# Kernel tuning notes

Measured on AMD Instinct MI355X. Metric: run time of the kernel, lower is better.

The kernel has to match this reference:

```python
import jax, jax.numpy as jnp
import numpy as np

N = 100000      # num zones (nodes)
E = 1600000     # num edges
IN = 16         # in_channels
HID = 128       # hidden_dim
HEADS = 4
C = HID // HEADS  # 32, per-head channels of gat1
NEG = 0.2       # PyG GATConv negative_slope default
LN_EPS = 1e-5


def setup_inputs() -> dict:
    key = jax.random.key(0)
    ks = jax.random.split(key, 14)
    x = jax.random.normal(ks[0], (N, IN), jnp.float32)
    edge_index = jax.random.randint(ks[1], (2, E), 0, N, dtype=jnp.int32)
    # --- GATConv layer 1: in=IN, heads=HEADS, out=C, concat=True ---
    W1 = jax.random.normal(ks[2], (IN, HEADS * C), jnp.float32) / np.sqrt(IN)
    a_src1 = jax.random.normal(ks[3], (HEADS, C), jnp.float32) / np.sqrt(C)
    a_dst1 = jax.random.normal(ks[4], (HEADS, C), jnp.float32) / np.sqrt(C)
    b1 = jnp.zeros((HEADS * C,), jnp.float32)
    # --- LayerNorm 1 ---
    g1 = jnp.ones((HID,), jnp.float32)
    beta1 = jnp.zeros((HID,), jnp.float32)
    # --- GATConv layer 2: in=HID, heads=1, out=HID, concat=False ---
    W2 = jax.random.normal(ks[5], (HID, HID), jnp.float32) / np.sqrt(HID)
    a_src2 = jax.random.normal(ks[6], (1, HID), jnp.float32) / np.sqrt(HID)
    a_dst2 = jax.random.normal(ks[7], (1, HID), jnp.float32) / np.sqrt(HID)
    b2 = jnp.zeros((HID,), jnp.float32)
    # --- LayerNorm 2 ---
    g2 = jnp.ones((HID,), jnp.float32)
    beta2 = jnp.zeros((HID,), jnp.float32)
    return dict(x=x, edge_index=edge_index, W1=W1, a_src1=a_src1, a_dst1=a_dst1,
                b1=b1, g1=g1, beta1=beta1, W2=W2, a_src2=a_src2, a_dst2=a_dst2,
                b2=b2, g2=g2, beta2=beta2)


def gat_conv(x, src, dst, W, a_src, a_dst, b, heads, ch, concat):
    """PyG GATConv (eval mode, no edge_attr), self-loops already in src/dst."""
    n = x.shape[0]
    h = (x @ W).reshape(n, heads, ch)                    # [N,H,C]
    alpha_src = jnp.einsum('nhc,hc->nh', h, a_src)       # [N,H]
    alpha_dst = jnp.einsum('nhc,hc->nh', h, a_dst)       # [N,H]
    e = jax.nn.leaky_relu(alpha_src[src] + alpha_dst[dst], NEG)  # [Etot,H]
    # segment softmax over destination node
    m = jax.ops.segment_max(e, dst, num_segments=n)      # [N,H]
    ex = jnp.exp(e - m[dst])
    denom = jax.ops.segment_sum(ex, dst, num_segments=n) # [N,H]
    alpha = ex / denom[dst]                              # [Etot,H]
    msg = h[src] * alpha[..., None]                      # [Etot,H,C]
    out = jax.ops.segment_sum(msg, dst, num_segments=n)  # [N,H,C]
    out = out.reshape(n, heads * ch) if concat else out.mean(axis=1)
    return out + b


def layer_norm(x, g, b):
    mu = x.mean(-1, keepdims=True)
    var = ((x - mu) ** 2).mean(-1, keepdims=True)
    return (x - mu) * jax.lax.rsqrt(var + LN_EPS) * g + b


def reference(x, edge_index, W1, a_src1, a_dst1, b1, g1, beta1,
              W2, a_src2, a_dst2, b2, g2, beta2):
    loops = jnp.arange(N, dtype=edge_index.dtype)
    src = jnp.concatenate([edge_index[0], loops])
    dst = jnp.concatenate([edge_index[1], loops])
    h = gat_conv(x, src, dst, W1, a_src1, a_dst1, b1, HEADS, C, concat=True)
    h = layer_norm(jax.nn.elu(h), g1, beta1)
    h = gat_conv(h, src, dst, W2, a_src2, a_dst2, b2, 1, HID, concat=False)
    h = layer_norm(jax.nn.elu(h), g2, beta2)
    return h
```

## Files before the change

kernel.cpp:

```cpp
#include <hip/hip_runtime.h>

#define IN_CH 16
#define HID 128
#define HEADS 4
#define NEG 0.2f
#define LN_EPS 1e-5f
#define BCAP 8192

typedef short bf16x8 __attribute__((ext_vector_type(8)));
typedef float f32x4 __attribute__((ext_vector_type(4)));

__device__ __forceinline__ float bf2f(unsigned short u) {
  return __uint_as_float(((unsigned)u) << 16);
}
__device__ __forceinline__ float bflo(unsigned u) {
  return __uint_as_float(u << 16);
}
__device__ __forceinline__ float bfhi(unsigned u) {
  return __uint_as_float(u & 0xffff0000u);
}
__device__ __forceinline__ unsigned short f2bf(float f) {
  unsigned u = __float_as_uint(f);
  unsigned r = (u + 0x7fffu + ((u >> 16) & 1u)) >> 16;
  return (unsigned short)r;
}
__device__ __forceinline__ float sb(unsigned v, int sh) {
  return (float)((int)(v << (24 - sh)) >> 24);
}

__global__ __launch_bounds__(128) void k_gemm1(
    const float* __restrict__ x, const float* __restrict__ W1,
    const float* __restrict__ a_src, const float* __restrict__ a_dst,
    signed char* __restrict__ hq, float* __restrict__ rec,
    float* __restrict__ adst, int N) {
  int n = blockIdx.x;
  int c = threadIdx.x;
  __shared__ float xs[IN_CH];
  __shared__ float wmax[2];
  if (c < IN_CH) xs[c] = x[n * IN_CH + c];
  __syncthreads();
  float acc = 0.f;
#pragma unroll
  for (int k = 0; k < IN_CH; ++k) acc += xs[k] * W1[k * HID + c];
  float av = acc * a_src[c];
  float dv = acc * a_dst[c];
#pragma unroll
  for (int o = 16; o > 0; o >>= 1) {
    av += __shfl_down(av, o, 32);
    dv += __shfl_down(dv, o, 32);
  }
  if ((c & 31) == 0) {
    rec[n * 8 + (c >> 5)] = av;
    adst[n * HEADS + (c >> 5)] = dv;
  }
  float m = fabsf(acc);
#pragma unroll
  for (int o = 32; o > 0; o >>= 1) m = fmaxf(m, __shfl_xor(m, o, 64));
  if ((c & 63) == 0) wmax[c >> 6] = m;
  __syncthreads();
  float mm = fmaxf(wmax[0], wmax[1]);
  float rs = (mm > 0.f) ? 127.f / mm : 0.f;
  hq[(size_t)n * HID + c] = (signed char)__float2int_rn(acc * rs);
  if (c == 0) rec[n * 8 + 4] = mm * (1.f / 127.f);
}

__global__ __launch_bounds__(256) void k_hist(
    const int* __restrict__ ei, int E, int Etot, int NBK, int NBLK,
    int* __restrict__ bcnt) {
  __shared__ int lh[512];
  int blk = blockIdx.x;
  for (int i = threadIdx.x; i < 512; i += 256) lh[i] = 0;
  __syncthreads();
  int s0 = blk * 8192, s1 = min(s0 + 8192, Etot);
  for (int e = s0 + threadIdx.x; e < s1; e += 256) {
    int d = (e < E) ? ei[E + e] : (e - E);
    atomicAdd(&lh[d >> 8], 1);
  }
  __syncthreads();
  for (int i = threadIdx.x; i < NBK; i += 256) bcnt[i * NBLK + blk] = lh[i];
}

__global__ __launch_bounds__(256) void k_scan1(
    const int* __restrict__ deg, int* __restrict__ part, int* __restrict__ aux,
    int N) {
  int i = blockIdx.x * 256 + threadIdx.x;
  int v = (i < N) ? deg[i] : 0;
  int lane = threadIdx.x & 63, w = threadIdx.x >> 6;
  int inc = v;
#pragma unroll
  for (int o = 1; o < 64; o <<= 1) {
    int t = __shfl_up(inc, o, 64);
    if (lane >= o) inc += t;
  }
  __shared__ int wsum[4];
  if (lane == 63) wsum[w] = inc;
  __syncthreads();
  int woff = 0;
#pragma unroll
  for (int k = 0; k < 4; ++k)
    if (k < w) woff += wsum[k];
  if (i < N) part[i] = woff + inc - v;
  if (threadIdx.x == 255) aux[blockIdx.x] = woff + inc;
}

__global__ __launch_bounds__(512) void k_scan2(int* __restrict__ aux, int nb) {
  int i = threadIdx.x;
  int v = (i < nb) ? aux[i] : 0;
  int lane = i & 63, w = i >> 6;
  int inc = v;
#pragma unroll
  for (int o = 1; o < 64; o <<= 1) {
    int t = __shfl_up(inc, o, 64);
    if (lane >= o) inc += t;
  }
  __shared__ int wsum[8];
  if (lane == 63) wsum[w] = inc;
  __syncthreads();
  int woff = 0;
#pragma unroll
  for (int k = 0; k < 8; ++k)
    if (k < w) woff += wsum[k];
  if (i < nb) aux[i] = woff + inc - v;
}

__global__ __launch_bounds__(256) void k_scan3g(
    const int* __restrict__ part, const int* __restrict__ aux,
    int* __restrict__ out, int M) {
  int i = blockIdx.x * 256 + threadIdx.x;
  if (i < M) out[i] = part[i] + aux[blockIdx.x];
}

__global__ __launch_bounds__(256) void k_bucket(
    const int* __restrict__ ei, const int* __restrict__ bpre, int E, int Etot,
    int NBK, int NBLK, unsigned* __restrict__ bbuf) {
  __shared__ int lc[512];
  int blk = blockIdx.x;
  for (int i = threadIdx.x; i < NBK; i += 256) lc[i] = bpre[i * NBLK + blk];
  __syncthreads();
  int s0 = blk * 8192, s1 = min(s0 + 8192, Etot);
  for (int e = s0 + threadIdx.x; e < s1; e += 256) {
    int d = (e < E) ? ei[E + e] : (e - E);
    int s = (e < E) ? ei[e] : d;
    int pos = atomicAdd(&lc[d >> 8], 1);
    bbuf[pos] = ((unsigned)s << 8) | (unsigned)(d & 255);
  }
}

__global__ __launch_bounds__(256) void k_build(
    const unsigned* __restrict__ bbuf, const int* __restrict__ bpre,
    int* __restrict__ rowstart, int* __restrict__ csr_src, int N, int Etot,
    int NBK, int NBLK) {
  __shared__ int ldeg[256], lcur[256], wsum[4];
  __shared__ int lout[BCAP];
  int bin = blockIdx.x;
  int base = bpre[bin * NBLK];
  int next = (bin + 1 < NBK) ? bpre[(bin + 1) * NBLK] : Etot;
  int cnt = next - base;
  if (cnt > BCAP) cnt = BCAP;
  int tid = threadIdx.x;
  ldeg[tid] = 0;
  __syncthreads();
  for (int i = tid; i < cnt; i += 256)
    atomicAdd(&ldeg[bbuf[base + i] & 255u], 1);
  __syncthreads();
  int v = ldeg[tid];
  int lane = tid & 63, wv = tid >> 6;
  int inc = v;
#pragma unroll
  for (int o = 1; o < 64; o <<= 1) {
    int t = __shfl_up(inc, o, 64);
    if (lane >= o) inc += t;
  }
  if (lane == 63) wsum[wv] = inc;
  __syncthreads();
  int woff = 0;
#pragma unroll
  for (int k = 0; k < 4; ++k)
    if (k < wv) woff += wsum[k];
  int pre = woff + inc - v;
  int node = bin * 256 + tid;
  if (node < N) rowstart[node] = base + pre;
  lcur[tid] = pre;
  __syncthreads();
  for (int i = tid; i < cnt; i += 256) {
    unsigned u = bbuf[base + i];
    int p = atomicAdd(&lcur[u & 255u], 1);
    lout[p] = (int)(u >> 8);
  }
  __syncthreads();
  for (int i = tid; i < cnt; i += 256) csr_src[base + i] = lout[i];
  if (bin == 0 && tid == 0) rowstart[N] = Etot;
}

__global__ __launch_bounds__(256) void k_agg1(
    const int* __restrict__ rowstart, const int* __restrict__ csr_src,
    const float* __restrict__ rec, const float* __restrict__ adst,
    const signed char* __restrict__ hq, const float* __restrict__ bias,
    const float* __restrict__ g, const float* __restrict__ beta,
    unsigned short* __restrict__ outb, int N) {
  int d = blockIdx.x * 16 + (threadIdx.x >> 4);
  if (d >= N) return;
  int lane = threadIdx.x & 15;
  int c0 = lane << 3;
  int hd = lane >> 2;
  float ad = adst[d * HEADS + hd];
  int beg = rowstart[d], end = rowstart[d + 1];
  float a0 = 0.f, a1 = 0.f, a2 = 0.f, a3 = 0.f;
  float a4 = 0.f, a5 = 0.f, a6 = 0.f, a7 = 0.f, wsum = 0.f;
  for (int i = beg; i < end; i += 8) {
    int s[8];
#pragma unroll
    for (int j = 0; j < 8; ++j) {
      int e = i + j;
      s[j] = csr_src[e < end ? e : end - 1];
    }
    float lg[8], sc[8];
    uint2 p[8];
#pragma unroll
    for (int j = 0; j < 8; ++j) {
      lg[j] = rec[s[j] * 8 + hd];
      sc[j] = rec[s[j] * 8 + 4];
    }
#pragma unroll
    for (int j = 0; j < 8; ++j)
      p[j] = *(const uint2*)(hq + (size_t)s[j] * HID + c0);
#pragma unroll
    for (int j = 0; j < 8; ++j) {
      float v = lg[j] + ad;
      v = v < 0.f ? NEG * v : v;
      float ex = __expf(v);
      float w = (i + j < end) ? ex : 0.f;
      wsum += w;
      float ws = w * sc[j];
      a0 += ws * sb(p[j].x, 0);
      a1 += ws * sb(p[j].x, 8);
      a2 += ws * sb(p[j].x, 16);
      a3 += ws * sb(p[j].x, 24);
      a4 += ws * sb(p[j].y, 0);
      a5 += ws * sb(p[j].y, 8);
      a6 += ws * sb(p[j].y, 16);
      a7 += ws * sb(p[j].y, 24);
    }
  }
  float rw = 1.f / wsum;
  float v0 = a0 * rw + bias[c0 + 0];
  float v1 = a1 * rw + bias[c0 + 1];
  float v2 = a2 * rw + bias[c0 + 2];
  float v3 = a3 * rw + bias[c0 + 3];
  float v4 = a4 * rw + bias[c0 + 4];
  float v5 = a5 * rw + bias[c0 + 5];
  float v6 = a6 * rw + bias[c0 + 6];
  float v7 = a7 * rw + bias[c0 + 7];
  v0 = v0 > 0.f ? v0 : (__expf(v0) - 1.f);
  v1 = v1 > 0.f ? v1 : (__expf(v1) - 1.f);
  v2 = v2 > 0.f ? v2 : (__expf(v2) - 1.f);
  v3 = v3 > 0.f ? v3 : (__expf(v3) - 1.f);
  v4 = v4 > 0.f ? v4 : (__expf(v4) - 1.f);
  v5 = v5 > 0.f ? v5 : (__expf(v5) - 1.f);
  v6 = v6 > 0.f ? v6 : (__expf(v6) - 1.f);
  v7 = v7 > 0.f ? v7 : (__expf(v7) - 1.f);
  float s1 = ((v0 + v1) + (v2 + v3)) + ((v4 + v5) + (v6 + v7));
  float s2 = ((v0 * v0 + v1 * v1) + (v2 * v2 + v3 * v3)) +
             ((v4 * v4 + v5 * v5) + (v6 * v6 + v7 * v7));
#pragma unroll
  for (int o = 8; o > 0; o >>= 1) {
    s1 += __shfl_down(s1, o, 16);
    s2 += __shfl_down(s2, o, 16);
  }
  s1 = __shfl(s1, 0, 16);
  s2 = __shfl(s2, 0, 16);
  float mu = s1 * (1.f / HID);
  float var = s2 * (1.f / HID) - mu * mu;
  float inv = rsqrtf(var + LN_EPS);
  ushort4 q0, q1;
  q0.x = f2bf((v0 - mu) * inv * g[c0 + 0] + beta[c0 + 0]);
  q0.y = f2bf((v1 - mu) * inv * g[c0 + 1] + beta[c0 + 1]);
  q0.z = f2bf((v2 - mu) * inv * g[c0 + 2] + beta[c0 + 2]);
  q0.w = f2bf((v3 - mu) * inv * g[c0 + 3] + beta[c0 + 3]);
  q1.x = f2bf((v4 - mu) * inv * g[c0 + 4] + beta[c0 + 4]);
  q1.y = f2bf((v5 - mu) * inv * g[c0 + 5] + beta[c0 + 5]);
  q1.z = f2bf((v6 - mu) * inv * g[c0 + 6] + beta[c0 + 6]);
  q1.w = f2bf((v7 - mu) * inv * g[c0 + 7] + beta[c0 + 7]);
  *(ushort4*)(outb + (size_t)d * HID + c0) = q0;
  *(ushort4*)(outb + (size_t)d * HID + c0 + 4) = q1;
}

__global__ __launch_bounds__(256) void k_agg2(
    const int* __restrict__ rowstart, const int* __restrict__ csr_src,
    const float* __restrict__ asrc, const float* __restrict__ adst,
    const unsigned short* __restrict__ hb, const float* __restrict__ bias,
    const float* __restrict__ g, const float* __restrict__ beta,
    float* __restrict__ out, int N) {
  int d = blockIdx.x * 16 + (threadIdx.x >> 4);
  if (d >= N) return;
  int lane = threadIdx.x & 15;
  int c0 = lane << 3;
  float ad = adst[d];
  int beg = rowstart[d], end = rowstart[d + 1];
  float a0 = 0.f, a1 = 0.f, a2 = 0.f, a3 = 0.f;
  float a4 = 0.f, a5 = 0.f, a6 = 0.f, a7 = 0.f, wsum = 0.f;
  for (int i = beg; i < end; i += 8) {
    int s[8];
#pragma unroll
    for (int j = 0; j < 8; ++j) {
      int e = i + j;
      s[j] = csr_src[e < end ? e : end - 1];
    }
    float lg[8];
    uint4 p[8];
#pragma unroll
    for (int j = 0; j < 8; ++j) lg[j] = asrc[s[j]];
#pragma unroll
    for (int j = 0; j < 8; ++j)
      p[j] = *(const uint4*)(hb + (size_t)s[j] * HID + c0);
    float wv[8];
#pragma unroll
    for (int j = 0; j < 8; ++j) {
      float v = lg[j] + ad;
      v = v < 0.f ? NEG * v : v;
      float ex = __expf(v);
      wv[j] = (i + j < end) ? ex : 0.f;
    }
    wsum += ((wv[0] + wv[1]) + (wv[2] + wv[3])) +
            ((wv[4] + wv[5]) + (wv[6] + wv[7]));
#pragma unroll
    for (int j = 0; j < 8; ++j) {
      a0 += wv[j] * bflo(p[j].x);
      a1 += wv[j] * bfhi(p[j].x);
      a2 += wv[j] * bflo(p[j].y);
      a3 += wv[j] * bfhi(p[j].y);
      a4 += wv[j] * bflo(p[j].z);
      a5 += wv[j] * bfhi(p[j].z);
      a6 += wv[j] * bflo(p[j].w);
      a7 += wv[j] * bfhi(p[j].w);
    }
  }
  float rw = 1.f / wsum;
  float v0 = a0 * rw + bias[c0 + 0];
  float v1 = a1 * rw + bias[c0 + 1];
  float v2 = a2 * rw + bias[c0 + 2];
  float v3 = a3 * rw + bias[c0 + 3];
  float v4 = a4 * rw + bias[c0 + 4];
  float v5 = a5 * rw + bias[c0 + 5];
  float v6 = a6 * rw + bias[c0 + 6];
  float v7 = a7 * rw + bias[c0 + 7];
  v0 = v0 > 0.f ? v0 : (__expf(v0) - 1.f);
  v1 = v1 > 0.f ? v1 : (__expf(v1) - 1.f);
  v2 = v2 > 0.f ? v2 : (__expf(v2) - 1.f);
  v3 = v3 > 0.f ? v3 : (__expf(v3) - 1.f);
  v4 = v4 > 0.f ? v4 : (__expf(v4) - 1.f);
  v5 = v5 > 0.f ? v5 : (__expf(v5) - 1.f);
  v6 = v6 > 0.f ? v6 : (__expf(v6) - 1.f);
  v7 = v7 > 0.f ? v7 : (__expf(v7) - 1.f);
  float s1 = ((v0 + v1) + (v2 + v3)) + ((v4 + v5) + (v6 + v7));
  float s2 = ((v0 * v0 + v1 * v1) + (v2 * v2 + v3 * v3)) +
             ((v4 * v4 + v5 * v5) + (v6 * v6 + v7 * v7));
#pragma unroll
  for (int o = 8; o > 0; o >>= 1) {
    s1 += __shfl_down(s1, o, 16);
    s2 += __shfl_down(s2, o, 16);
  }
  s1 = __shfl(s1, 0, 16);
  s2 = __shfl(s2, 0, 16);
  float mu = s1 * (1.f / HID);
  float var = s2 * (1.f / HID) - mu * mu;
  float inv = rsqrtf(var + LN_EPS);
  float4 o0, o1;
  o0.x = (v0 - mu) * inv * g[c0 + 0] + beta[c0 + 0];
  o0.y = (v1 - mu) * inv * g[c0 + 1] + beta[c0 + 1];
  o0.z = (v2 - mu) * inv * g[c0 + 2] + beta[c0 + 2];
  o0.w = (v3 - mu) * inv * g[c0 + 3] + beta[c0 + 3];
  o1.x = (v4 - mu) * inv * g[c0 + 4] + beta[c0 + 4];
  o1.y = (v5 - mu) * inv * g[c0 + 5] + beta[c0 + 5];
  o1.z = (v6 - mu) * inv * g[c0 + 6] + beta[c0 + 6];
  o1.w = (v7 - mu) * inv * g[c0 + 7] + beta[c0 + 7];
  *(float4*)(out + (size_t)d * HID + c0) = o0;
  *(float4*)(out + (size_t)d * HID + c0 + 4) = o1;
}

__global__ __launch_bounds__(256) void k_w2pack(
    const float* __restrict__ W2, unsigned short* __restrict__ w2hi,
    unsigned short* __restrict__ w2lo) {
  int idx = blockIdx.x * 256 + threadIdx.x;
  int i = idx & 7;
  int lane = (idx >> 3) & 63;
  int t = (idx >> 9) & 7;
  int kb = idx >> 12;
  int k = kb * 32 + (lane >> 4) * 8 + i;
  int c = t * 16 + (lane & 15);
  float w = W2[k * HID + c];
  unsigned short hi = f2bf(w);
  float res = w - bf2f(hi);
  w2hi[idx] = hi;
  w2lo[idx] = f2bf(res);
}

__global__ __launch_bounds__(256) void k_gemm2m(
    const unsigned short* __restrict__ x2b,
    const unsigned short* __restrict__ w2hi,
    const unsigned short* __restrict__ w2lo,
    const float* __restrict__ a_src, const float* __restrict__ a_dst,
    unsigned short* __restrict__ h2b, float* __restrict__ asrc,
    float* __restrict__ adst, int N) {
  __shared__ float cs[4][16][132];
  int w = threadIdx.x >> 6;
  int l = threadIdx.x & 63;
  int n0 = blockIdx.x * 128 + w * 32;
  int m = l & 15;
  int kg = l >> 4;
  int naA = n0 + m;
  if (naA >= N) naA = N - 1;
  int naB = n0 + 16 + m;
  if (naB >= N) naB = N - 1;
  const unsigned short* xA = x2b + (size_t)naA * HID + kg * 8;
  const unsigned short* xB = x2b + (size_t)naB * HID + kg * 8;
  f32x4 accA[8] = {};
  f32x4 accB[8] = {};
#pragma unroll
  for (int kb = 0; kb < 4; ++kb) {
    bf16x8 aA = *(const bf16x8*)(xA + kb * 32);
    bf16x8 aB = *(const bf16x8*)(xB + kb * 32);
#pragma unroll
    for (int t = 0; t < 8; ++t) {
      bf16x8 bl = *(const bf16x8*)(w2lo + ((kb * 8 + t) * 64 + l) * 8);
      bf16x8 bh = *(const bf16x8*)(w2hi + ((kb * 8 + t) * 64 + l) * 8);
      accA[t] = __builtin_amdgcn_mfma_f32_16x16x32_bf16(aA, bl, accA[t], 0, 0, 0);
      accA[t] = __builtin_amdgcn_mfma_f32_16x16x32_bf16(aA, bh, accA[t], 0, 0, 0);
      accB[t] = __builtin_amdgcn_mfma_f32_16x16x32_bf16(aB, bl, accB[t], 0, 0, 0);
      accB[t] = __builtin_amdgcn_mfma_f32_16x16x32_bf16(aB, bh, accB[t], 0, 0, 0);
    }
  }
  auto epilog = [&](const f32x4(&acc)[8], int noff) {
#pragma unroll
    for (int t = 0; t < 8; ++t)
#pragma unroll
      for (int j = 0; j < 4; ++j) cs[w][kg * 4 + j][t * 16 + m] = acc[t][j];
    __syncthreads();
    int r2 = l & 15;
    int q = l >> 4;
    int n = n0 + noff + r2;
    if (n < N) {
      const float* rowp = &cs[w][r2][0];
      float pa = 0.f, pd = 0.f;
#pragma unroll
      for (int j = 0; j < 8; ++j) {
        int cc = q * 32 + j * 4;
        float4 v = *(const float4*)(rowp + cc);
        float4 as = *(const float4*)(a_src + cc);
        float4 av = *(const float4*)(a_dst + cc);
        pa += v.x * as.x + v.y * as.y + v.z * as.z + v.w * as.w;
        pd += v.x * av.x + v.y * av.y + v.z * av.z + v.w * av.w;
        ushort4 ob;
        ob.x = f2bf(v.x);
        ob.y = f2bf(v.y);
        ob.z = f2bf(v.z);
        ob.w = f2bf(v.w);
        *(ushort4*)(h2b + (size_t)n * HID + cc) = ob;
      }
      pa += __shfl_xor(pa, 16, 64);
      pa += __shfl_xor(pa, 32, 64);
      pd += __shfl_xor(pd, 16, 64);
      pd += __shfl_xor(pd, 32, 64);
      if (q == 0) {
        asrc[n] = pa;
        adst[n] = pd;
      }
    }
    __syncthreads();
  };
  epilog(accA, 0);
  epilog(accB, 16);
}

extern "C" void kernel_launch(void* const* d_in, const int* in_sizes, int n_in,
                              void* d_out, int out_size, void* d_ws, size_t ws_size,
                              hipStream_t stream) {
  const float* x      = (const float*)d_in[0];
  const int*   ei     = (const int*)d_in[1];
  const float* W1     = (const float*)d_in[2];
  const float* a_src1 = (const float*)d_in[3];
  const float* a_dst1 = (const float*)d_in[4];
  const float* b1     = (const float*)d_in[5];
  const float* g1     = (const float*)d_in[6];
  const float* beta1  = (const float*)d_in[7];
  const float* W2     = (const float*)d_in[8];
  const float* a_src2 = (const float*)d_in[9];
  const float* a_dst2 = (const float*)d_in[10];
  const float* b2     = (const float*)d_in[11];
  const float* g2     = (const float*)d_in[12];
  const float* beta2  = (const float*)d_in[13];
  float* out = (float*)d_out;

  const int N = in_sizes[0] / IN_CH;
  const int E = in_sizes[1] / 2;
  const int Etot = E + N;

  const int NBK = (N + 255) >> 8;
  const int NBLK = (Etot + 8191) >> 13;
  const int M = NBK * NBLK;
  const int Mblk = (M + 255) / 256;

  unsigned char* U = (unsigned char*)d_ws;
  signed char* hq = (signed char*)U;
  float* rec = (float*)(U + (size_t)N * HID);
  unsigned short* x2b =
      (unsigned short*)(U + (size_t)N * HID + (size_t)N * 32);
  unsigned short* h2b = x2b + (size_t)N * HID;
  float* adst1 = (float*)(h2b + (size_t)N * HID);
  float* asrc2 = adst1 + (size_t)N * HEADS;
  float* adst2 = asrc2 + N;
  int* rowstart = (int*)(adst2 + N);
  int* aux      = rowstart + N + 4;
  int* bcnt     = aux + 1024;
  int* bpart    = bcnt + M;
  int* bpre     = bpart + M;
  unsigned* bbuf = (unsigned*)(bpre + M);
  int* csr_src  = (int*)(bbuf + Etot);
  unsigned short* w2hi = (unsigned short*)(csr_src + Etot);
  unsigned short* w2lo = w2hi + 16384;

  k_w2pack<<<64, 256, 0, stream>>>(W2, w2hi, w2lo);

  k_hist<<<NBLK, 256, 0, stream>>>(ei, E, Etot, NBK, NBLK, bcnt);
  k_scan1<<<Mblk, 256, 0, stream>>>(bcnt, bpart, aux, M);
  k_scan2<<<1, 512, 0, stream>>>(aux, Mblk);
  k_scan3g<<<Mblk, 256, 0, stream>>>(bpart, aux, bpre, M);
  k_bucket<<<NBLK, 256, 0, stream>>>(ei, bpre, E, Etot, NBK, NBLK, bbuf);
  k_build<<<NBK, 256, 0, stream>>>(bbuf, bpre, rowstart, csr_src, N, Etot,
                                   NBK, NBLK);

  k_gemm1<<<N, 128, 0, stream>>>(x, W1, a_src1, a_dst1, hq, rec, adst1, N);
  k_agg1<<<(N + 15) / 16, 256, 0, stream>>>(rowstart, csr_src, rec, adst1, hq,
                                            b1, g1, beta1, x2b, N);

  k_gemm2m<<<(N + 127) / 128, 256, 0, stream>>>(x2b, w2hi, w2lo, a_src2,
                                                a_dst2, h2b, asrc2, adst2, N);
  k_agg2<<<(N + 15) / 16, 256, 0, stream>>>(rowstart, csr_src, asrc2, adst2,
                                            h2b, b2, g2, beta2, out, N);
}
```

Baseline: 357.4 us.

## Quantize layer-2 features to int8 with per-node scale and batch gemm1 nodes

Layer-2 projected features are now stored as int8 with a per-node absmax scale, packed alongside the source attention logit in a float2. This replaces bf16 storage and halves the bytes gathered per edge in the second aggregation. Separately, gemm1 now handles 8 nodes per block, with W1 staged in shared memory and float4 math, instead of one 128-thread block per node. The int8 quantization lowers precision of the layer-2 messages, which risks larger numerical error in the output.

```diff
diff --git a/kernel.cpp b/kernel.cpp
--- a/kernel.cpp
+++ b/kernel.cpp
@@ -28,40 +28,64 @@
   return (float)((int)(v << (24 - sh)) >> 24);
 }
 
-__global__ __launch_bounds__(128) void k_gemm1(
+__global__ __launch_bounds__(256) void k_gemm1(
     const float* __restrict__ x, const float* __restrict__ W1,
     const float* __restrict__ a_src, const float* __restrict__ a_dst,
     signed char* __restrict__ hq, float* __restrict__ rec,
     float* __restrict__ adst, int N) {
-  int n = blockIdx.x;
-  int c = threadIdx.x;
-  __shared__ float xs[IN_CH];
-  __shared__ float wmax[2];
-  if (c < IN_CH) xs[c] = x[n * IN_CH + c];
-  __syncthreads();
-  float acc = 0.f;
-#pragma unroll
-  for (int k = 0; k < IN_CH; ++k) acc += xs[k] * W1[k * HID + c];
-  float av = acc * a_src[c];
-  float dv = acc * a_dst[c];
-#pragma unroll
-  for (int o = 16; o > 0; o >>= 1) {
-    av += __shfl_down(av, o, 32);
-    dv += __shfl_down(dv, o, 32);
-  }
-  if ((c & 31) == 0) {
-    rec[n * 8 + (c >> 5)] = av;
-    adst[n * HEADS + (c >> 5)] = dv;
-  }
-  float m = fabsf(acc);
-#pragma unroll
-  for (int o = 32; o > 0; o >>= 1) m = fmaxf(m, __shfl_xor(m, o, 64));
-  if ((c & 63) == 0) wmax[c >> 6] = m;
-  __syncthreads();
-  float mm = fmaxf(wmax[0], wmax[1]);
-  float rs = (mm > 0.f) ? 127.f / mm : 0.f;
-  hq[(size_t)n * HID + c] = (signed char)__float2int_rn(acc * rs);
-  if (c == 0) rec[n * 8 + 4] = mm * (1.f / 127.f);
+  __shared__ float w1s[IN_CH][HID];
+  __shared__ float xsh[8][IN_CH];
+  int tid = threadIdx.x;
+  int nb = blockIdx.x * 8;
+  for (int i = tid; i < IN_CH * HID; i += 256) ((float*)w1s)[i] = W1[i];
+  if (tid < 128) {
+    int nl = tid >> 4, k = tid & 15;
+    int n = nb + nl;
+    xsh[nl][k] = (n < N) ? x[n * IN_CH + k] : 0.f;
+  }
+  __syncthreads();
+  int nl = tid >> 5;
+  int l32 = tid & 31;
+  int c0 = l32 << 2;
+  int n = nb + nl;
+  float4 acc = make_float4(0.f, 0.f, 0.f, 0.f);
+#pragma unroll
+  for (int k = 0; k < IN_CH; ++k) {
+    float xv = xsh[nl][k];
+    float4 wv = *(const float4*)(&w1s[k][c0]);
+    acc.x += xv * wv.x;
+    acc.y += xv * wv.y;
+    acc.z += xv * wv.z;
+    acc.w += xv * wv.w;
+  }
+  float4 as4 = *(const float4*)(a_src + c0);
+  float4 ad4 = *(const float4*)(a_dst + c0);
+  float av = acc.x * as4.x + acc.y * as4.y + acc.z * as4.z + acc.w * as4.w;
+  float dv = acc.x * ad4.x + acc.y * ad4.y + acc.z * ad4.z + acc.w * ad4.w;
+  av += __shfl_xor(av, 1);
+  av += __shfl_xor(av, 2);
+  av += __shfl_xor(av, 4);
+  dv += __shfl_xor(dv, 1);
+  dv += __shfl_xor(dv, 2);
+  dv += __shfl_xor(dv, 4);
+  float m = fmaxf(fmaxf(fabsf(acc.x), fabsf(acc.y)),
+                  fmaxf(fabsf(acc.z), fabsf(acc.w)));
+#pragma unroll
+  for (int o = 1; o < 32; o <<= 1) m = fmaxf(m, __shfl_xor(m, o));
+  if (n < N) {
+    float rs = (m > 0.f) ? 127.f / m : 0.f;
+    int b0 = __float2int_rn(acc.x * rs) & 255;
+    int b1 = __float2int_rn(acc.y * rs) & 255;
+    int b2 = __float2int_rn(acc.z * rs) & 255;
+    int b3 = __float2int_rn(acc.w * rs) & 255;
+    *(unsigned*)(hq + (size_t)n * HID + c0) =
+        (unsigned)(b0 | (b1 << 8) | (b2 << 16) | (b3 << 24));
+    if ((l32 & 7) == 0) {
+      rec[n * 8 + (l32 >> 3)] = av;
+      adst[n * HEADS + (l32 >> 3)] = dv;
+    }
+    if (l32 == 0) rec[n * 8 + 4] = m * (1.f / 127.f);
+  }
 }
 
 __global__ __launch_bounds__(256) void k_hist(
@@ -287,8 +311,8 @@
 
 __global__ __launch_bounds__(256) void k_agg2(
     const int* __restrict__ rowstart, const int* __restrict__ csr_src,
-    const float* __restrict__ asrc, const float* __restrict__ adst,
-    const unsigned short* __restrict__ hb, const float* __restrict__ bias,
+    const float2* __restrict__ rec2, const float* __restrict__ adst,
+    const signed char* __restrict__ hq2, const float* __restrict__ bias,
     const float* __restrict__ g, const float* __restrict__ beta,
     float* __restrict__ out, int N) {
   int d = blockIdx.x * 16 + (threadIdx.x >> 4);
@@ -306,33 +330,29 @@
       int e = i + j;
       s[j] = csr_src[e < end ? e : end - 1];
     }
-    float lg[8];
-    uint4 p[8];
-#pragma unroll
-    for (int j = 0; j < 8; ++j) lg[j] = asrc[s[j]];
+    float2 r[8];
+    uint2 p[8];
+#pragma unroll
+    for (int j = 0; j < 8; ++j) r[j] = rec2[s[j]];
 #pragma unroll
     for (int j = 0; j < 8; ++j)
-      p[j] = *(const uint4*)(hb + (size_t)s[j] * HID + c0);
-    float wv[8];
+      p[j] = *(const uint2*)(hq2 + (size_t)s[j] * HID + c0);
 #pragma unroll
     for (int j = 0; j < 8; ++j) {
-      float v = lg[j] + ad;
+      float v = r[j].x + ad;
       v = v < 0.f ? NEG * v : v;
       float ex = __expf(v);
-      wv[j] = (i + j < end) ? ex : 0.f;
-    }
-    wsum += ((wv[0] + wv[1]) + (wv[2] + wv[3])) +
-            ((wv[4] + wv[5]) + (wv[6] + wv[7]));
-#pragma unroll
-    for (int j = 0; j < 8; ++j) {
-      a0 += wv[j] * bflo(p[j].x);
-      a1 += wv[j] * bfhi(p[j].x);
-      a2 += wv[j] * bflo(p[j].y);
-      a3 += wv[j] * bfhi(p[j].y);
-      a4 += wv[j] * bflo(p[j].z);
-      a5 += wv[j] * bfhi(p[j].z);
-      a6 += wv[j] * bflo(p[j].w);
-      a7 += wv[j] * bfhi(p[j].w);
+      float w = (i + j < end) ? ex : 0.f;
+      wsum += w;
+      float ws = w * r[j].y;
+      a0 += ws * sb(p[j].x, 0);
+      a1 += ws * sb(p[j].x, 8);
+      a2 += ws * sb(p[j].x, 16);
+      a3 += ws * sb(p[j].x, 24);
+      a4 += ws * sb(p[j].y, 0);
+      a5 += ws * sb(p[j].y, 8);
+      a6 += ws * sb(p[j].y, 16);
+      a7 += ws * sb(p[j].y, 24);
     }
   }
   float rw = 1.f / wsum;
@@ -400,7 +420,7 @@
     const unsigned short* __restrict__ w2hi,
     const unsigned short* __restrict__ w2lo,
     const float* __restrict__ a_src, const float* __restrict__ a_dst,
-    unsigned short* __restrict__ h2b, float* __restrict__ asrc,
+    signed char* __restrict__ hq2, float2* __restrict__ rec2,
     float* __restrict__ adst, int N) {
   __shared__ float cs[4][16][132];
   int w = threadIdx.x >> 6;
@@ -439,30 +459,43 @@
     int r2 = l & 15;
     int q = l >> 4;
     int n = n0 + noff + r2;
+    const float* rowp = &cs[w][r2][0];
+    float4 v[8];
+    float pa = 0.f, pd = 0.f, mx = 0.f;
+#pragma unroll
+    for (int j = 0; j < 8; ++j) {
+      int cc = q * 32 + j * 4;
+      v[j] = *(const float4*)(rowp + cc);
+      float4 as = *(const float4*)(a_src + cc);
+      float4 av = *(const float4*)(a_dst + cc);
+      pa += v[j].x * as.x + v[j].y * as.y + v[j].z * as.z + v[j].w * as.w;
+      pd += v[j].x * av.x + v[j].y * av.y + v[j].z * av.z + v[j].w * av.w;
+      mx = fmaxf(mx, fmaxf(fmaxf(fabsf(v[j].x), fabsf(v[j].y)),
+                           fmaxf(fabsf(v[j].z), fabsf(v[j].w))));
+    }
+    pa += __shfl_xor(pa, 16);
+    pa += __shfl_xor(pa, 32);
+    pd += __shfl_xor(pd, 16);
+    pd += __shfl_xor(pd, 32);
+    mx = fmaxf(mx, __shfl_xor(mx, 16));
+    mx = fmaxf(mx, __shfl_xor(mx, 32));
     if (n < N) {
-      const float* rowp = &cs[w][r2][0];
-      float pa = 0.f, pd = 0.f;
+      float rs = (mx > 0.f) ? 127.f / mx : 0.f;
+      unsigned u[8];
 #pragma unroll
       for (int j = 0; j < 8; ++j) {
-        int cc = q * 32 + j * 4;
-        float4 v = *(const float4*)(rowp + cc);
-        float4 as = *(const float4*)(a_src + cc);
-        float4 av = *(const float4*)(a_dst + cc);
-        pa += v.x * as.x + v.y * as.y + v.z * as.z + v.w * as.w;
-        pd += v.x * av.x + v.y * av.y + v.z * av.z + v.w * av.w;
-        ushort4 ob;
-        ob.x = f2bf(v.x);
-        ob.y = f2bf(v.y);
-        ob.z = f2bf(v.z);
-        ob.w = f2bf(v.w);
-        *(ushort4*)(h2b + (size_t)n * HID + cc) = ob;
+        int b0 = __float2int_rn(v[j].x * rs) & 255;
+        int b1 = __float2int_rn(v[j].y * rs) & 255;
+        int b2 = __float2int_rn(v[j].z * rs) & 255;
+        int b3 = __float2int_rn(v[j].w * rs) & 255;
+        u[j] = (unsigned)(b0 | (b1 << 8) | (b2 << 16) | (b3 << 24));
       }
-      pa += __shfl_xor(pa, 16, 64);
-      pa += __shfl_xor(pa, 32, 64);
-      pd += __shfl_xor(pd, 16, 64);
-      pd += __shfl_xor(pd, 32, 64);
+      *(uint4*)(hq2 + (size_t)n * HID + q * 32) =
+          make_uint4(u[0], u[1], u[2], u[3]);
+      *(uint4*)(hq2 + (size_t)n * HID + q * 32 + 16) =
+          make_uint4(u[4], u[5], u[6], u[7]);
       if (q == 0) {
-        asrc[n] = pa;
+        rec2[n] = make_float2(pa, mx * (1.f / 127.f));
         adst[n] = pd;
       }
     }
@@ -505,10 +538,10 @@
   float* rec = (float*)(U + (size_t)N * HID);
   unsigned short* x2b =
       (unsigned short*)(U + (size_t)N * HID + (size_t)N * 32);
-  unsigned short* h2b = x2b + (size_t)N * HID;
-  float* adst1 = (float*)(h2b + (size_t)N * HID);
-  float* asrc2 = adst1 + (size_t)N * HEADS;
-  float* adst2 = asrc2 + N;
+  signed char* hq2 = (signed char*)(x2b + (size_t)N * HID);
+  float2* rec2 = (float2*)(hq2 + (size_t)N * HID);
+  float* adst1 = (float*)(rec2 + N);
+  float* adst2 = adst1 + (size_t)N * HEADS;
   int* rowstart = (int*)(adst2 + N);
   int* aux      = rowstart + N + 4;
   int* bcnt     = aux + 1024;
@@ -529,12 +562,13 @@
   k_build<<<NBK, 256, 0, stream>>>(bbuf, bpre, rowstart, csr_src, N, Etot,
                                    NBK, NBLK);
 
-  k_gemm1<<<N, 128, 0, stream>>>(x, W1, a_src1, a_dst1, hq, rec, adst1, N);
+  k_gemm1<<<(N + 7) / 8, 256, 0, stream>>>(x, W1, a_src1, a_dst1, hq, rec,
+                                           adst1, N);
   k_agg1<<<(N + 15) / 16, 256, 0, stream>>>(rowstart, csr_src, rec, adst1, hq,
                                             b1, g1, beta1, x2b, N);
 
   k_gemm2m<<<(N + 127) / 128, 256, 0, stream>>>(x2b, w2hi, w2lo, a_src2,
-                                                a_dst2, h2b, asrc2, adst2, N);
-  k_agg2<<<(N + 15) / 16, 256, 0, stream>>>(rowstart, csr_src, asrc2, adst2,
-                                            h2b, b2, g2, beta2, out, N);
-}
+                                                a_dst2, hq2, rec2, adst2, N);
+  k_agg2<<<(N + 15) / 16, 256, 0, stream>>>(rowstart, csr_src, rec2, adst2,
+                                            hq2, b2, g2, beta2, out, N);
+}
```

Result: faster. 304.9 us (-14.7%).
